# Kernel optimization log

Measured on AMD Instinct MI355X. Metric: run time of the kernel, lower is better.

The kernel has to match this reference:

```python
import jax, jax.numpy as jnp
import numpy as np

N_NODES = 100000
N_EDGES = 1600000
DIM = 64
N_GRAPHS = 1000


def setup_inputs() -> dict:
    key = jax.random.key(0)
    ks = jax.random.split(key, 6)
    s = 1.0 / np.sqrt(DIM)
    x = jax.random.normal(ks[0], (N_NODES, DIM), dtype=jnp.float32)
    edge_index = jax.random.randint(ks[1], (2, N_EDGES), 0, N_NODES, dtype=jnp.int64)
    batch = jnp.sort(jax.random.randint(ks[2], (N_NODES,), 0, N_GRAPHS, dtype=jnp.int64))
    W1 = jax.random.normal(ks[3], (DIM, DIM), dtype=jnp.float32) * s
    b1 = jnp.zeros((DIM,), jnp.float32)
    W2 = jax.random.normal(ks[4], (DIM, DIM), dtype=jnp.float32) * s
    b2 = jnp.zeros((DIM,), jnp.float32)
    return {"x": x, "W1": W1, "b1": b1, "W2": W2, "b2": b2,
            "edge_index": edge_index, "batch": batch}


def reference(x, W1, b1, W2, b2, edge_index, batch):
    n = x.shape[0]
    loop = jnp.arange(n, dtype=edge_index.dtype)
    src = jnp.concatenate([edge_index[0], loop])  # [E+N] with self-loops
    dst = jnp.concatenate([edge_index[1], loop])
    # symmetric GCN normalization: deg^{-1/2}[src] * deg^{-1/2}[dst]
    deg = jax.ops.segment_sum(jnp.ones(src.shape[0], x.dtype), dst, num_segments=n)
    dinv = jax.lax.rsqrt(jnp.maximum(deg, 1.0))  # deg >= 1 due to self-loops
    norm = (dinv[src] * dinv[dst])[:, None]      # [E+N, 1]

    def gcn(h, W, b):
        h = h @ W                                  # transform first (smaller dim path)
        msg = h[src] * norm                        # gather + normalize
        return jax.ops.segment_sum(msg, dst, num_segments=n) + b

    h = jax.nn.relu(gcn(x, W1, b1))
    # dropout: eval mode -> identity
    h = jax.nn.relu(gcn(h, W2, b2))

    counts = jax.ops.segment_sum(jnp.ones((n,), x.dtype), batch, num_segments=N_GRAPHS)
    pooled = jax.ops.segment_sum(h, batch, num_segments=N_GRAPHS)
    return pooled / jnp.maximum(counts, 1.0)[:, None]
```

## Files before the change

kernel.cpp:

```cpp
#include <hip/hip_runtime.h>
#include <hip/hip_fp16.h>

#define DIM 64
#define BIN_SHIFT 7
#define BINSZ 128
#define MAXBINS 1024
#define PB 512

typedef __attribute__((ext_vector_type(2))) float floatx2;
typedef __attribute__((ext_vector_type(4))) float f32x4;
typedef __attribute__((ext_vector_type(8))) _Float16 f16x8;
typedef __attribute__((ext_vector_type(4))) _Float16 f16x4;


__global__ __launch_bounds__(256) void k_zero(int* __restrict__ bintot,
                                              float* __restrict__ out,
                                              int NB, int GD) {
    int i = blockIdx.x * 256 + threadIdx.x;
    if (i < NB) bintot[i] = 0;
    for (int j = i; j < GD; j += gridDim.x * 256) out[j] = 0.f;
}


__global__ __launch_bounds__(256) void k_hist2(const int* __restrict__ dst,
                                               int* __restrict__ bintot, int E, int NB) {
    __shared__ int h[MAXBINS];
    for (int i = threadIdx.x; i < NB; i += 256) h[i] = 0;
    __syncthreads();
    int per = (E + PB - 1) / PB;
    int e0 = blockIdx.x * per;
    int e1 = e0 + per; if (e1 > E) e1 = E;
    for (int e = e0 + (int)threadIdx.x; e < e1; e += 256)
        atomicAdd(&h[dst[e] >> BIN_SHIFT], 1);
    __syncthreads();
    for (int i = threadIdx.x; i < NB; i += 256)
        if (h[i]) atomicAdd(&bintot[i], h[i]);
}


__global__ __launch_bounds__(256) void k_scan782(const int* __restrict__ bintot,
                                                 int* __restrict__ binoff,
                                                 int* __restrict__ bincur, int NB, int E) {
    __shared__ int ws[4];
    int tid = threadIdx.x;
    int j0 = tid * 4;
    int v[4]; int sum = 0;
#pragma unroll
    for (int t = 0; t < 4; ++t) {
        int j = j0 + t;
        int x = (j < NB) ? bintot[j] : 0;
        v[t] = sum; sum += x;
    }
    int lane = tid & 63, wv = tid >> 6;
    int x = sum;
#pragma unroll
    for (int d = 1; d < 64; d <<= 1) {
        int t = __shfl_up(x, d);
        if (lane >= d) x += t;
    }
    if (lane == 63) ws[wv] = x;
    __syncthreads();
    int prefix = 0;
    for (int w = 0; w < wv; ++w) prefix += ws[w];
    int ex = prefix + x - sum;
#pragma unroll
    for (int t = 0; t < 4; ++t) {
        int j = j0 + t;
        if (j < NB) { binoff[j] = ex + v[t]; bincur[j] = ex + v[t]; }
    }
    if (tid == 255) binoff[NB] = prefix + x;
}


__global__ __launch_bounds__(256) void k_bucket2(const int* __restrict__ src,
                                                 const int* __restrict__ dst,
                                                 int* __restrict__ bincur,
                                                 int* __restrict__ bkt, int E, int NB) {
    __shared__ int cnt_[MAXBINS], base_[MAXBINS];
    int tid = threadIdx.x;
    for (int i = tid; i < NB; i += 256) cnt_[i] = 0;
    __syncthreads();
    int per = (E + PB - 1) / PB;
    int e0 = blockIdx.x * per;
    int e1 = e0 + per; if (e1 > E) e1 = E;
    for (int e = e0 + tid; e < e1; e += 256)
        atomicAdd(&cnt_[dst[e] >> BIN_SHIFT], 1);
    __syncthreads();
    for (int i = tid; i < NB; i += 256) {
        int c = cnt_[i];
        base_[i] = c ? atomicAdd(&bincur[i], c) : 0;
        cnt_[i] = 0;
    }
    __syncthreads();
    for (int e = e0 + tid; e < e1; e += 256) {
        int d = dst[e];
        int b = d >> BIN_SHIFT;
        int pos = base_[b] + atomicAdd(&cnt_[b], 1);
        bkt[pos] = src[e] | ((d & (BINSZ - 1)) << 24);
    }
}


__global__ __launch_bounds__(256) void k_binsort(const int* __restrict__ bkt,
                                                 const int* __restrict__ binoff,
                                                 int* __restrict__ csr,
                                                 int* __restrict__ off,
                                                 float* __restrict__ dinv,
                                                 const int* __restrict__ batch,
                                                 int* __restrict__ goff,
                                                 int N, int G, int E, int NB) {
    __shared__ int cnt[BINSZ], bas[BINSZ], cur[BINSZ];
    __shared__ int wsum[4];
    int tid = threadIdx.x;
    int b = blockIdx.x;
    int s0 = binoff[b];
    int s1 = binoff[b + 1];
    if (tid < BINSZ) { cnt[tid] = 0; cur[tid] = 0; }
    __syncthreads();
    for (int i = s0 + tid; i < s1; i += 256)
        atomicAdd(&cnt[(bkt[i] >> 24) & (BINSZ - 1)], 1);
    __syncthreads();
    int my = (tid < BINSZ) ? cnt[tid] : 0;
    int lane = tid & 63, wv = tid >> 6;
    int x = my;
#pragma unroll
    for (int d = 1; d < 64; d <<= 1) {
        int t = __shfl_up(x, d);
        if (lane >= d) x += t;
    }
    if (lane == 63) wsum[wv] = x;
    __syncthreads();
    int prefix = 0;
    for (int w = 0; w < wv; ++w) prefix += wsum[w];
    int ex = x + prefix - my;
    if (tid < BINSZ) {
        bas[tid] = ex;
        int v = (b << BIN_SHIFT) + tid;
        if (v < N) {
            off[v] = s0 + ex;
            dinv[v] = rsqrtf((float)(my + 1));
            if (v == N - 1) off[N] = E;
            int bb = batch[v];
            int prev = (v == 0) ? -1 : batch[v - 1];
            for (int g = prev + 1; g <= bb; ++g) goff[g] = v;
            if (v == N - 1)
                for (int g = bb + 1; g <= G; ++g) goff[g] = N;
        }
    }
    __syncthreads();
    for (int i = s0 + tid; i < s1; i += 256) {
        int p = bkt[i];
        int lo = (p >> 24) & (BINSZ - 1);
        int li = atomicAdd(&cur[lo], 1);
        csr[s0 + bas[lo] + li] = p & 0xFFFFFF;
    }
}


__global__ __launch_bounds__(256) void k_gemm(const float* __restrict__ X,
                                              const float* __restrict__ W,
                                              const float* __restrict__ dinv,
                                              unsigned int* __restrict__ Y8, int N) {
    __shared__ float Os[16 * 68];
    int tid = threadIdx.x;
    int lane = tid & 63, w = tid >> 6;
    int m = lane & 15, g = lane >> 4;
    int row0 = blockIdx.x * 16;
    int row = row0 + m;

    f16x8 B0, B1;
    {
        int n = (w << 4) + m;
        const float* wp = W + (g << 3) * 64 + n;
#pragma unroll
        for (int j = 0; j < 8; ++j) B0[j] = (_Float16)wp[j * 64];
        wp += 32 * 64;
#pragma unroll
        for (int j = 0; j < 8; ++j) B1[j] = (_Float16)wp[j * 64];
    }
    f16x8 A0, A1;
    {
        float4 u0 = make_float4(0.f, 0.f, 0.f, 0.f), u1 = u0, u2 = u0, u3 = u0;
        if (row < N) {
            const float* xp = X + (size_t)row * DIM + (g << 3);
            u0 = *(const float4*)(xp);
            u1 = *(const float4*)(xp + 4);
            u2 = *(const float4*)(xp + 32);
            u3 = *(const float4*)(xp + 36);
        }
        A0[0] = (_Float16)u0.x; A0[1] = (_Float16)u0.y; A0[2] = (_Float16)u0.z; A0[3] = (_Float16)u0.w;
        A0[4] = (_Float16)u1.x; A0[5] = (_Float16)u1.y; A0[6] = (_Float16)u1.z; A0[7] = (_Float16)u1.w;
        A1[0] = (_Float16)u2.x; A1[1] = (_Float16)u2.y; A1[2] = (_Float16)u2.z; A1[3] = (_Float16)u2.w;
        A1[4] = (_Float16)u3.x; A1[5] = (_Float16)u3.y; A1[6] = (_Float16)u3.z; A1[7] = (_Float16)u3.w;
    }
    f32x4 acc = {0.f, 0.f, 0.f, 0.f};
    acc = __builtin_amdgcn_mfma_f32_16x16x32_f16(A0, B0, acc, 0, 0, 0);
    acc = __builtin_amdgcn_mfma_f32_16x16x32_f16(A1, B1, acc, 0, 0, 0);
#pragma unroll
    for (int j = 0; j < 4; ++j)
        Os[((g << 2) + j) * 68 + (w << 4) + m] = acc[j];
    __syncthreads();

    int r = tid >> 4, c = tid & 15;
    int orow = row0 + r;
    if (orow < N) {
        float4 o = *(const float4*)(Os + r * 68 + (c << 2));
        float s = dinv[orow];
        int p = 0;
        p = __builtin_amdgcn_cvt_pk_fp8_f32(o.x * s, o.y * s, p, false);
        p = __builtin_amdgcn_cvt_pk_fp8_f32(o.z * s, o.w * s, p, true);
        Y8[(size_t)orow * 16 + c] = (unsigned int)p;
    } else if (orow == N) {
        Y8[(size_t)orow * 16 + c] = 0u;
    }
}


__device__ __forceinline__ float4 gather_rows(const unsigned int* __restrict__ hs8,
                                              const int* __restrict__ csr,
                                              int k0, int k1, int v, int l, int gw4,
                                              int N) {
    float4 a0, a1, a2, a3;
    {
        unsigned int u = hs8[(unsigned)((v << 4) | l)];
        floatx2 f0 = __builtin_amdgcn_cvt_pk_f32_fp8((int)u, false);
        floatx2 f1 = __builtin_amdgcn_cvt_pk_f32_fp8((int)u, true);
        a0 = make_float4(f0.x, f0.y, f1.x, f1.y);
        a1 = make_float4(0.f, 0.f, 0.f, 0.f);
        a2 = make_float4(0.f, 0.f, 0.f, 0.f);
        a3 = make_float4(0.f, 0.f, 0.f, 0.f);
    }
    for (int kb = k0; kb < k1; kb += 16) {
        int rem = k1 - kb;
        int idx = (l < rem) ? csr[kb + l] : N;
        unsigned uu[16];
#pragma unroll
        for (int t = 0; t < 16; ++t) {
            int s = __shfl(idx, gw4 + t);
            uu[t] = hs8[(unsigned)((s << 4) | l)];
        }
#pragma unroll
        for (int t = 0; t < 16; t += 4) {
            floatx2 q0 = __builtin_amdgcn_cvt_pk_f32_fp8((int)uu[t + 0], false);
            floatx2 q1 = __builtin_amdgcn_cvt_pk_f32_fp8((int)uu[t + 0], true);
            floatx2 q2 = __builtin_amdgcn_cvt_pk_f32_fp8((int)uu[t + 1], false);
            floatx2 q3 = __builtin_amdgcn_cvt_pk_f32_fp8((int)uu[t + 1], true);
            floatx2 q4 = __builtin_amdgcn_cvt_pk_f32_fp8((int)uu[t + 2], false);
            floatx2 q5 = __builtin_amdgcn_cvt_pk_f32_fp8((int)uu[t + 2], true);
            floatx2 q6 = __builtin_amdgcn_cvt_pk_f32_fp8((int)uu[t + 3], false);
            floatx2 q7 = __builtin_amdgcn_cvt_pk_f32_fp8((int)uu[t + 3], true);
            a0.x += q0.x; a0.y += q0.y; a0.z += q1.x; a0.w += q1.y;
            a1.x += q2.x; a1.y += q2.y; a1.z += q3.x; a1.w += q3.y;
            a2.x += q4.x; a2.y += q4.y; a2.z += q5.x; a2.w += q5.y;
            a3.x += q6.x; a3.y += q6.y; a3.z += q7.x; a3.w += q7.y;
        }
    }
    return make_float4(a0.x + a1.x + a2.x + a3.x,
                       a0.y + a1.y + a2.y + a3.y,
                       a0.z + a1.z + a2.z + a3.z,
                       a0.w + a1.w + a2.w + a3.w);
}


__global__ __launch_bounds__(256) void k_gather_gemm(const unsigned int* __restrict__ hs8,
                                                     const int* __restrict__ csr,
                                                     const int* __restrict__ off,
                                                     const float* __restrict__ dinv,
                                                     const float* __restrict__ bias,
                                                     const float* __restrict__ W,
                                                     unsigned int* __restrict__ hs_out,
                                                     int N) {
    __shared__ _Float16 Xs[16 * 72];
    __shared__ float Os[16 * 68];
    int tid = threadIdx.x;
    int r = tid >> 4, l = tid & 15;
    int lane = tid & 63, w = tid >> 6;
    int m = lane & 15, g = lane >> 4;
    int gw4 = (r & 3) << 4;
    int v = blockIdx.x * 16 + r;

    f16x8 B0, B1;
    {
        int n = (w << 4) + m;
        const float* wp = W + (g << 3) * 64 + n;
#pragma unroll
        for (int j = 0; j < 8; ++j) B0[j] = (_Float16)wp[j * 64];
        wp += 32 * 64;
#pragma unroll
        for (int j = 0; j < 8; ++j) B1[j] = (_Float16)wp[j * 64];
    }
    if (blockIdx.x == 0 && tid < 16)
        hs_out[(size_t)N * 16 + tid] = 0u;

    float dv = 0.f;
    float4 h = make_float4(0.f, 0.f, 0.f, 0.f);
    if (v < N) {
        dv = dinv[v];
        float4 bv = ((const float4*)bias)[l];
        float4 acc = gather_rows(hs8, csr, off[v], off[v + 1], v, l, gw4, N);
        h.x = fmaxf(acc.x * dv + bv.x, 0.f);
        h.y = fmaxf(acc.y * dv + bv.y, 0.f);
        h.z = fmaxf(acc.z * dv + bv.z, 0.f);
        h.w = fmaxf(acc.w * dv + bv.w, 0.f);
    }
    {
        f16x4 hv;
        hv[0] = (_Float16)h.x; hv[1] = (_Float16)h.y;
        hv[2] = (_Float16)h.z; hv[3] = (_Float16)h.w;
        *(f16x4*)(Xs + r * 72 + (l << 2)) = hv;
    }
    __syncthreads();

    f16x8 A0 = *(const f16x8*)(Xs + m * 72 + (g << 3));
    f16x8 A1 = *(const f16x8*)(Xs + m * 72 + 32 + (g << 3));
    f32x4 acc2 = {0.f, 0.f, 0.f, 0.f};
    acc2 = __builtin_amdgcn_mfma_f32_16x16x32_f16(A0, B0, acc2, 0, 0, 0);
    acc2 = __builtin_amdgcn_mfma_f32_16x16x32_f16(A1, B1, acc2, 0, 0, 0);
#pragma unroll
    for (int j = 0; j < 4; ++j)
        Os[((g << 2) + j) * 68 + (w << 4) + m] = acc2[j];
    __syncthreads();

    if (v < N) {
        float4 o = *(const float4*)(Os + r * 68 + (l << 2));
        int p = 0;
        p = __builtin_amdgcn_cvt_pk_fp8_f32(o.x * dv, o.y * dv, p, false);
        p = __builtin_amdgcn_cvt_pk_fp8_f32(o.z * dv, o.w * dv, p, true);
        hs_out[(size_t)v * 16 + l] = (unsigned int)p;
    }
}


__global__ __launch_bounds__(256) void k_gather_pool(const unsigned int* __restrict__ hs8,
                                                     const int* __restrict__ csr,
                                                     const int* __restrict__ off,
                                                     const float* __restrict__ dinv,
                                                     const float* __restrict__ bias,
                                                     const int* __restrict__ batch,
                                                     const int* __restrict__ goff,
                                                     float* __restrict__ out, int N) {
    __shared__ float vals[16][68];
    __shared__ int gid[16];
    int tid = threadIdx.x;
    int r = tid >> 4, l = tid & 15;
    int gw4 = (r & 3) << 4;
    int v = blockIdx.x * 16 + r;

    float4 val = make_float4(0.f, 0.f, 0.f, 0.f);
    int g = -1;
    if (v < N) {
        g = batch[v];
        float dv = dinv[v];
        float4 bv = ((const float4*)bias)[l];
        float4 acc = gather_rows(hs8, csr, off[v], off[v + 1], v, l, gw4, N);
        float inv = 1.0f / (float)(goff[g + 1] - goff[g]);
        val.x = fmaxf(acc.x * dv + bv.x, 0.f) * inv;
        val.y = fmaxf(acc.y * dv + bv.y, 0.f) * inv;
        val.z = fmaxf(acc.z * dv + bv.z, 0.f) * inv;
        val.w = fmaxf(acc.w * dv + bv.w, 0.f) * inv;
    }
    *(float4*)(&vals[r][l << 2]) = val;
    if (l == 0) gid[r] = g;
    __syncthreads();

    if (v < N) {
        bool leader = (r == 0) || (gid[r - 1] != g);
        if (leader) {
            float4 sacc = val;
            for (int rr = r + 1; rr < 16 && gid[rr] == g; ++rr) {
                float4 t = *(const float4*)(&vals[rr][l << 2]);
                sacc.x += t.x; sacc.y += t.y; sacc.z += t.z; sacc.w += t.w;
            }
            float* op = out + (size_t)g * DIM + (l << 2);
            atomicAdd(op + 0, sacc.x);
            atomicAdd(op + 1, sacc.y);
            atomicAdd(op + 2, sacc.z);
            atomicAdd(op + 3, sacc.w);
        }
    }
}


static inline int cdiv(int a, int b) { return (a + b - 1) / b; }

extern "C" void kernel_launch(void* const* d_in, const int* in_sizes, int n_in,
                              void* d_out, int out_size, void* d_ws, size_t ws_size,
                              hipStream_t stream) {
    const float* x   = (const float*)d_in[0];
    const float* W1  = (const float*)d_in[1];
    const float* b1  = (const float*)d_in[2];
    const float* W2  = (const float*)d_in[3];
    const float* b2  = (const float*)d_in[4];
    const int*   ei  = (const int*)d_in[5];
    const int*   bat = (const int*)d_in[6];

    const int N = in_sizes[0] / DIM;
    const int E = in_sizes[5] / 2;
    const int G = out_size / DIM;
    const int NB = cdiv(N, BINSZ);
    const int* src = ei;
    const int* dst = ei + E;
    float* out = (float*)d_out;

    __half* hs1    = (__half*)d_ws;
    __half* hs2    = hs1 + (size_t)(N + 1) * DIM;
    float*  dinv   = (float*)(hs2 + (size_t)(N + 1) * DIM);
    int*    off    = (int*)(dinv + N);
    int*    goff   = off + (N + 1);
    int*    bintot = goff + (G + 1);
    int*    binoff = bintot + MAXBINS;
    int*    bincur = binoff + (MAXBINS + 1);
    int*    csr    = bincur + MAXBINS;
    int*    bkt    = (int*)hs1;

    k_zero<<<256, 256, 0, stream>>>(bintot, out, NB, G * DIM);
    k_hist2<<<PB, 256, 0, stream>>>(dst, bintot, E, NB);
    k_scan782<<<1, 256, 0, stream>>>(bintot, binoff, bincur, NB, E);
    k_bucket2<<<PB, 256, 0, stream>>>(src, dst, bincur, bkt, E, NB);
    k_binsort<<<NB, 256, 0, stream>>>(bkt, binoff, csr, off, dinv, bat, goff, N, G, E, NB);

    k_gemm<<<cdiv(N + 1, 16), 256, 0, stream>>>(x, W1, dinv, (unsigned int*)hs1, N);

    k_gather_gemm<<<cdiv(N, 16), 256, 0, stream>>>((const unsigned int*)hs1, csr, off,
                                                   dinv, b1, W2, (unsigned int*)hs2, N);

    k_gather_pool<<<cdiv(N, 16), 256, 0, stream>>>((const unsigned int*)hs2, csr, off,
                                                   dinv, b2, bat, goff, out, N);
}
```

Baseline: 218.9 us.

## Fuse histogram and bucketing into one pass with per-block local bin segments

Merges the global histogram and bucket-scatter kernels into one kernel. Each block counts its edges per bin, scans locally, and writes them into its own contiguous slice of the bucket array, recording a per-block offset and length for every bin. The bin-sort kernel then reads each bin's pieces from the 512 block slices through these offset/length tables instead of one contiguous global range. This removes one full pass over the dst array, the global cursor atomics, and a kernel launch, but the bin-sort now walks the pieces serially per thread, with strided loads and possible load imbalance.

```diff
diff --git a/kernel.cpp b/kernel.cpp
--- a/kernel.cpp
+++ b/kernel.cpp
@@ -15,32 +15,77 @@
 
 __global__ __launch_bounds__(256) void k_zero(int* __restrict__ bintot,
                                               float* __restrict__ out,
-                                              int NB, int GD) {
+                                              int NBZ, int GD) {
     int i = blockIdx.x * 256 + threadIdx.x;
-    if (i < NB) bintot[i] = 0;
-    for (int j = i; j < GD; j += gridDim.x * 256) out[j] = 0.f;
-}
-
-
-__global__ __launch_bounds__(256) void k_hist2(const int* __restrict__ dst,
-                                               int* __restrict__ bintot, int E, int NB) {
-    __shared__ int h[MAXBINS];
-    for (int i = threadIdx.x; i < NB; i += 256) h[i] = 0;
+    int stride = gridDim.x * 256;
+    for (int j = i; j < NBZ; j += stride) bintot[j] = 0;
+    for (int j = i; j < GD; j += stride) out[j] = 0.f;
+}
+
+
+__global__ __launch_bounds__(256) void k_bucket3(const int* __restrict__ src,
+                                                 const int* __restrict__ dst,
+                                                 int* __restrict__ bintot,
+                                                 int* __restrict__ C,
+                                                 int* __restrict__ LEN,
+                                                 int* __restrict__ bkt, int E, int NB) {
+    __shared__ int cnt[MAXBINS], bas[MAXBINS];
+    __shared__ int ws[4];
+    int tid = threadIdx.x, blk = blockIdx.x;
+    for (int i = tid; i < NB; i += 256) cnt[i] = 0;
     __syncthreads();
     int per = (E + PB - 1) / PB;
-    int e0 = blockIdx.x * per;
+    int e0 = blk * per;
     int e1 = e0 + per; if (e1 > E) e1 = E;
-    for (int e = e0 + (int)threadIdx.x; e < e1; e += 256)
-        atomicAdd(&h[dst[e] >> BIN_SHIFT], 1);
-    __syncthreads();
-    for (int i = threadIdx.x; i < NB; i += 256)
-        if (h[i]) atomicAdd(&bintot[i], h[i]);
+    for (int e = e0 + tid; e < e1; e += 256)
+        atomicAdd(&cnt[dst[e] >> BIN_SHIFT], 1);
+    __syncthreads();
+    int j0 = tid * 4;
+    int v[4]; int sum = 0;
+#pragma unroll
+    for (int t = 0; t < 4; ++t) {
+        int j = j0 + t;
+        int x = (j < NB) ? cnt[j] : 0;
+        v[t] = sum; sum += x;
+    }
+    int lane = tid & 63, wv = tid >> 6;
+    int x = sum;
+#pragma unroll
+    for (int d = 1; d < 64; d <<= 1) {
+        int t = __shfl_up(x, d);
+        if (lane >= d) x += t;
+    }
+    if (lane == 63) ws[wv] = x;
+    __syncthreads();
+    int prefix = 0;
+    for (int w = 0; w < wv; ++w) prefix += ws[w];
+    int ex = prefix + x - sum;
+#pragma unroll
+    for (int t = 0; t < 4; ++t) {
+        int j = j0 + t;
+        if (j < NB) bas[j] = ex + v[t];
+    }
+    __syncthreads();
+    int nbb = blk * NB;
+    for (int i = tid; i < NB; i += 256) {
+        int c = cnt[i];
+        C[nbb + i] = bas[i];
+        LEN[nbb + i] = c;
+        if (c) atomicAdd(&bintot[i], c);
+        cnt[i] = 0;
+    }
+    __syncthreads();
+    for (int e = e0 + tid; e < e1; e += 256) {
+        int d = dst[e];
+        int bb = d >> BIN_SHIFT;
+        int pos = bas[bb] + atomicAdd(&cnt[bb], 1);
+        bkt[e0 + pos] = src[e] | ((d & (BINSZ - 1)) << 24);
+    }
 }
 
 
 __global__ __launch_bounds__(256) void k_scan782(const int* __restrict__ bintot,
-                                                 int* __restrict__ binoff,
-                                                 int* __restrict__ bincur, int NB, int E) {
+                                                 int* __restrict__ binoff, int NB, int E) {
     __shared__ int ws[4];
     int tid = threadIdx.x;
     int j0 = tid * 4;
@@ -66,59 +111,37 @@
 #pragma unroll
     for (int t = 0; t < 4; ++t) {
         int j = j0 + t;
-        if (j < NB) { binoff[j] = ex + v[t]; bincur[j] = ex + v[t]; }
+        if (j < NB) binoff[j] = ex + v[t];
     }
     if (tid == 255) binoff[NB] = prefix + x;
 }
 
 
-__global__ __launch_bounds__(256) void k_bucket2(const int* __restrict__ src,
-                                                 const int* __restrict__ dst,
-                                                 int* __restrict__ bincur,
-                                                 int* __restrict__ bkt, int E, int NB) {
-    __shared__ int cnt_[MAXBINS], base_[MAXBINS];
-    int tid = threadIdx.x;
-    for (int i = tid; i < NB; i += 256) cnt_[i] = 0;
-    __syncthreads();
-    int per = (E + PB - 1) / PB;
-    int e0 = blockIdx.x * per;
-    int e1 = e0 + per; if (e1 > E) e1 = E;
-    for (int e = e0 + tid; e < e1; e += 256)
-        atomicAdd(&cnt_[dst[e] >> BIN_SHIFT], 1);
-    __syncthreads();
-    for (int i = tid; i < NB; i += 256) {
-        int c = cnt_[i];
-        base_[i] = c ? atomicAdd(&bincur[i], c) : 0;
-        cnt_[i] = 0;
-    }
-    __syncthreads();
-    for (int e = e0 + tid; e < e1; e += 256) {
-        int d = dst[e];
-        int b = d >> BIN_SHIFT;
-        int pos = base_[b] + atomicAdd(&cnt_[b], 1);
-        bkt[pos] = src[e] | ((d & (BINSZ - 1)) << 24);
-    }
-}
-
-
-__global__ __launch_bounds__(256) void k_binsort(const int* __restrict__ bkt,
-                                                 const int* __restrict__ binoff,
-                                                 int* __restrict__ csr,
-                                                 int* __restrict__ off,
-                                                 float* __restrict__ dinv,
-                                                 const int* __restrict__ batch,
-                                                 int* __restrict__ goff,
-                                                 int N, int G, int E, int NB) {
+__global__ __launch_bounds__(256) void k_binsort2(const int* __restrict__ bkt,
+                                                  const int* __restrict__ C,
+                                                  const int* __restrict__ LEN,
+                                                  const int* __restrict__ binoff,
+                                                  int* __restrict__ csr,
+                                                  int* __restrict__ off,
+                                                  float* __restrict__ dinv,
+                                                  const int* __restrict__ batch,
+                                                  int* __restrict__ goff,
+                                                  int N, int G, int E, int NB) {
     __shared__ int cnt[BINSZ], bas[BINSZ], cur[BINSZ];
     __shared__ int wsum[4];
     int tid = threadIdx.x;
     int b = blockIdx.x;
+    int per = (E + PB - 1) / PB;
     int s0 = binoff[b];
-    int s1 = binoff[b + 1];
     if (tid < BINSZ) { cnt[tid] = 0; cur[tid] = 0; }
     __syncthreads();
-    for (int i = s0 + tid; i < s1; i += 256)
-        atomicAdd(&cnt[(bkt[i] >> 24) & (BINSZ - 1)], 1);
+    int f0 = tid * 2;
+    int ca = C[f0 * NB + b],       lna = LEN[f0 * NB + b];
+    int cb = C[(f0 + 1) * NB + b], lnb = LEN[(f0 + 1) * NB + b];
+    const int* pa  = bkt + f0 * per + ca;
+    const int* pb_ = bkt + (f0 + 1) * per + cb;
+    for (int j = 0; j < lna; ++j) atomicAdd(&cnt[(pa[j]  >> 24) & (BINSZ - 1)], 1);
+    for (int j = 0; j < lnb; ++j) atomicAdd(&cnt[(pb_[j] >> 24) & (BINSZ - 1)], 1);
     __syncthreads();
     int my = (tid < BINSZ) ? cnt[tid] : 0;
     int lane = tid & 63, wv = tid >> 6;
@@ -148,8 +171,14 @@
         }
     }
     __syncthreads();
-    for (int i = s0 + tid; i < s1; i += 256) {
-        int p = bkt[i];
+    for (int j = 0; j < lna; ++j) {
+        int p = pa[j];
+        int lo = (p >> 24) & (BINSZ - 1);
+        int li = atomicAdd(&cur[lo], 1);
+        csr[s0 + bas[lo] + li] = p & 0xFFFFFF;
+    }
+    for (int j = 0; j < lnb; ++j) {
+        int p = pb_[j];
         int lo = (p >> 24) & (BINSZ - 1);
         int li = atomicAdd(&cur[lo], 1);
         csr[s0 + bas[lo] + li] = p & 0xFFFFFF;
@@ -409,15 +438,16 @@
     int*    goff   = off + (N + 1);
     int*    bintot = goff + (G + 1);
     int*    binoff = bintot + MAXBINS;
-    int*    bincur = binoff + (MAXBINS + 1);
-    int*    csr    = bincur + MAXBINS;
+    int*    C      = binoff + (MAXBINS + 1);
+    int*    LEN    = C + (size_t)PB * NB;
+    int*    csr    = LEN + (size_t)PB * NB;
     int*    bkt    = (int*)hs1;
 
-    k_zero<<<256, 256, 0, stream>>>(bintot, out, NB, G * DIM);
-    k_hist2<<<PB, 256, 0, stream>>>(dst, bintot, E, NB);
-    k_scan782<<<1, 256, 0, stream>>>(bintot, binoff, bincur, NB, E);
-    k_bucket2<<<PB, 256, 0, stream>>>(src, dst, bincur, bkt, E, NB);
-    k_binsort<<<NB, 256, 0, stream>>>(bkt, binoff, csr, off, dinv, bat, goff, N, G, E, NB);
+    k_zero<<<256, 256, 0, stream>>>(bintot, out, MAXBINS, G * DIM);
+    k_bucket3<<<PB, 256, 0, stream>>>(src, dst, bintot, C, LEN, bkt, E, NB);
+    k_scan782<<<1, 256, 0, stream>>>(bintot, binoff, NB, E);
+    k_binsort2<<<NB, 256, 0, stream>>>(bkt, C, LEN, binoff, csr, off, dinv, bat,
+                                       goff, N, G, E, NB);
 
     k_gemm<<<cdiv(N + 1, 16), 256, 0, stream>>>(x, W1, dinv, (unsigned int*)hs1, N);
 
```

New measurement: 219.4 us. Within noise of the previous version (+0.2%).
